# Kernel tuning notes

Measured on AMD Instinct MI355X. Metric: run time of the kernel, lower is better.

## Reference

```python
import jax, jax.numpy as jnp
import numpy as np

HIDDEN = 768
NUM_HEADS = 12
HEAD_DIM = HIDDEN // NUM_HEADS
NUM_SELECTED = 64
SCALE = 1.0 / np.sqrt(HEAD_DIM)


def setup_inputs() -> dict:
    key = jax.random.key(0)
    k0, k1, k2, k3, k4 = jax.random.split(key, 5)
    B, S = 1, 2048
    inputs = jax.random.normal(k0, (B, S, HIDDEN), dtype=jnp.float32)
    # nn.Linear weights, stored as [out, in]; applied as x @ W.T
    Wq = jax.random.normal(k1, (HIDDEN, HIDDEN), dtype=jnp.float32) * 0.02
    Wk = jax.random.normal(k2, (HIDDEN, HIDDEN), dtype=jnp.float32) * 0.02
    Wv = jax.random.normal(k3, (HIDDEN, HIDDEN), dtype=jnp.float32) * 0.02
    Wo = jax.random.normal(k4, (HIDDEN, HIDDEN), dtype=jnp.float32) * 0.02
    return {"inputs": inputs, "Wq": Wq, "Wk": Wk, "Wv": Wv, "Wo": Wo}


def reference(inputs, Wq, Wk, Wv, Wo):
    B, S, H = inputs.shape
    K = NUM_SELECTED
    pos = jnp.arange(S)
    window_starts = jnp.clip(pos + 1 - K, 0, None)                      # [S]
    sel = window_starts[:, None] + jnp.arange(K)[None, :]               # [S, K]
    sel = jnp.clip(sel, 0, S - 1)
    causal_mask = sel <= pos[:, None]                                   # [S, K]

    # Per-token linear projections; gathering after the (per-token) linear is
    # mathematically identical to the original gather-then-project.
    q = inputs @ Wq.T                                                   # [B,S,H]
    k_full = inputs @ Wk.T                                              # [B,S,H]
    v_full = inputs @ Wv.T                                              # [B,S,H]

    k = k_full[:, sel]                                                  # [B,S,K,H]
    v = v_full[:, sel]                                                  # [B,S,K,H]

    q = q.reshape(B, S, NUM_HEADS, HEAD_DIM)                            # [B,S,n,d]
    k = k.reshape(B, S, K, NUM_HEADS, HEAD_DIM)                         # [B,S,K,n,d]
    v = v.reshape(B, S, K, NUM_HEADS, HEAD_DIM)

    scores = jnp.einsum("bsnd,bsknd->bnsk", q, k) * SCALE               # [B,n,S,K]
    scores = jnp.where(causal_mask[None, None], scores, -jnp.inf)
    weights = jax.nn.softmax(scores, axis=-1)                           # [B,n,S,K]

    out = jnp.einsum("bnsk,bsknd->bsnd", weights, v)                    # [B,S,n,d]
    out = out.reshape(B, S, H)
    return out @ Wo.T
```

## Files before the change

### kernel.cpp

```cpp
#include <hip/hip_runtime.h>
#include <stdint.h>

#define S_LEN   2048
#define HIDDEN  768
#define NHEADS  12
#define QKV_LD  2304
#define NW      589824

#define REP_CONV 8

typedef __attribute__((ext_vector_type(8))) short short8;
typedef __attribute__((ext_vector_type(4))) float f32x4;

typedef const __attribute__((address_space(1))) void* gas_ptr;
typedef __attribute__((address_space(3))) void* las_ptr;

__device__ __forceinline__ short f2b(float f) {
    union { float f; uint32_t u; } v; v.f = f;
    uint32_t u = v.u;
    uint32_t r = (u + 0x7FFFu + ((u >> 16) & 1u)) >> 16;
    return (short)r;
}

__global__ __launch_bounds__(256)
void convert_all(const float* __restrict__ X,
                 const float* __restrict__ Wq, const float* __restrict__ Wk,
                 const float* __restrict__ Wv, const float* __restrict__ Wo,
                 short* __restrict__ Xb, short* __restrict__ Wqkvb,
                 short* __restrict__ Wob) {
    const int NX4 = 393216, NW4 = 147456, TOT = 983040;
    for (int rep = 0; rep < REP_CONV; ++rep) {
        for (int idx = blockIdx.x * 256 + threadIdx.x; idx < TOT; idx += 1024 * 256) {
            const float* src; short* dst; int e;
            if (idx < NX4) {
                src = X; dst = Xb; e = idx * 4;
            } else {
                int j = idx - NX4;
                int wb = j / NW4, lb = j % NW4;
                src = wb == 0 ? Wq : wb == 1 ? Wk : wb == 2 ? Wv : Wo;
                dst = wb < 3 ? Wqkvb + wb * NW : Wob;
                e = lb * 4;
            }
            float4 v = *(const float4*)(src + e);
            *(short4*)(dst + e) = make_short4(f2b(v.x), f2b(v.y), f2b(v.z), f2b(v.w));
        }
        asm volatile("" ::: "memory");
    }
}

template<int OUT_BF16>
__device__ __forceinline__ void gemm64x128(const short* __restrict__ A,
    const short* __restrict__ B, void* __restrict__ Cv,
    int bm, int bn, int ldc) {
    __shared__ short sA[2][64 * 64];
    __shared__ short sB[2][128 * 64];

    const int tid = threadIdx.x, lane = tid & 63, w = tid >> 6;
    const int wr = w >> 1, wc = w & 1;

    f32x4 acc[2][4] = {};

    auto stage = [&](int buf, int k0) {
        #pragma unroll
        for (int c = 0; c < 2; ++c) {
            int r = w * 16 + c * 8 + (lane >> 3);
            int scb = ((lane & 7) * 16) ^ ((r & 7) << 4);
            const char* gp = (const char*)(A + (size_t)(bm * 64 + r) * 768 + k0) + scb;
            __builtin_amdgcn_global_load_lds((gas_ptr)gp,
                (las_ptr)((char*)&sA[buf][0] + w * 2048 + c * 1024), 16, 0, 0);
        }
        #pragma unroll
        for (int c = 0; c < 4; ++c) {
            int r = w * 32 + c * 8 + (lane >> 3);
            int scb = ((lane & 7) * 16) ^ ((r & 7) << 4);
            const char* gp = (const char*)(B + (size_t)(bn * 128 + r) * 768 + k0) + scb;
            __builtin_amdgcn_global_load_lds((gas_ptr)gp,
                (las_ptr)((char*)&sB[buf][0] + w * 4096 + c * 1024), 16, 0, 0);
        }
    };

    stage(0, 0);
    __syncthreads();
    int cur = 0;
    for (int t = 0; t < 12; ++t) {
        if (t < 11) stage(cur ^ 1, (t + 1) * 64);
        #pragma unroll
        for (int kh = 0; kh < 2; ++kh) {
            const int kb = kh * 64 + ((lane >> 4) << 4);
            short8 av[2], bv[4];
            #pragma unroll
            for (int mi = 0; mi < 2; ++mi) {
                int row = wr * 32 + mi * 16 + (lane & 15);
                av[mi] = *(const short8*)((const char*)&sA[cur][0] + row * 128 + (kb ^ ((row & 7) << 4)));
            }
            #pragma unroll
            for (int ni = 0; ni < 4; ++ni) {
                int row = wc * 64 + ni * 16 + (lane & 15);
                bv[ni] = *(const short8*)((const char*)&sB[cur][0] + row * 128 + (kb ^ ((row & 7) << 4)));
            }
            #pragma unroll
            for (int mi = 0; mi < 2; ++mi)
                #pragma unroll
                for (int ni = 0; ni < 4; ++ni)
                    acc[mi][ni] = __builtin_amdgcn_mfma_f32_16x16x32_bf16(
                        av[mi], bv[ni], acc[mi][ni], 0, 0, 0);
        }
        __syncthreads();
        cur ^= 1;
    }

    const int crow0 = bm * 64 + wr * 32;
    const int ccol0 = bn * 128 + wc * 64;
    #pragma unroll
    for (int mi = 0; mi < 2; ++mi)
        #pragma unroll
        for (int ni = 0; ni < 4; ++ni)
            #pragma unroll
            for (int r = 0; r < 4; ++r) {
                int grow = crow0 + mi * 16 + ((lane >> 4) << 2) + r;
                int gcol = ccol0 + ni * 16 + (lane & 15);
                if (OUT_BF16)
                    ((short*)Cv)[(size_t)grow * ldc + gcol] = f2b(acc[mi][ni][r]);
                else
                    ((float*)Cv)[(size_t)grow * ldc + gcol] = acc[mi][ni][r];
            }
}

__global__ __launch_bounds__(256)
void gemm_qkv(const short* __restrict__ Xb, const short* __restrict__ Wqkvb,
              short* __restrict__ C) {
    const int x = blockIdx.x & 7, i = blockIdx.x >> 3;
    const int bm = (x >> 1) * 8 + i / 9;
    const int bn = (x & 1) * 9 + i % 9;
    gemm64x128<1>(Xb, Wqkvb, C, bm, bn, QKV_LD);
}

__global__ __launch_bounds__(256)
void gemm_out(const short* __restrict__ A, const short* __restrict__ Wob,
              float* __restrict__ C) {
    const int bid = blockIdx.x;
    const int sw = (bid & 7) * 24 + (bid >> 3);
    gemm64x128<0>(A, Wob, C, sw / 6, sw % 6, HIDDEN);
}

__global__ __launch_bounds__(256)
void attn_mfma(const short* __restrict__ QKV, short* __restrict__ O) {
    __shared__ short sK[128 * 64];
    __shared__ short sVt[64 * 128];
    __shared__ short sP[4][16 * 128];

    const int bid = blockIdx.x;
    const int task = (bid & 7) * 48 + (bid >> 3);
    const int h = task % NHEADS;
    const int s0 = (task / NHEADS) * 64;
    const int tid = threadIdx.x, lane = tid & 63, w = tid >> 6;

    #pragma unroll
    for (int c = 0; c < 4; ++c) {
        int r = (w * 4 + c) * 8 + (lane >> 3);
        int gr = s0 - 64 + r; if (gr < 0) gr = 0;
        int scb = ((lane & 7) * 16) ^ ((r & 7) << 4);
        const char* gp = (const char*)(QKV + (size_t)gr * QKV_LD + 768 + h * 64) + scb;
        __builtin_amdgcn_global_load_lds((gas_ptr)gp,
            (las_ptr)((char*)sK + (w * 4 + c) * 1024), 16, 0, 0);
    }
    {
        const int d0 = (tid & 7) * 8;
        const int kbase = (tid >> 3) * 4;
        short8 v[4];
        #pragma unroll
        for (int i = 0; i < 4; ++i) {
            int gr = s0 - 64 + kbase + i; if (gr < 0) gr = 0;
            v[i] = *(const short8*)(QKV + (size_t)gr * QKV_LD + 1536 + h * 64 + d0);
        }
        #pragma unroll
        for (int j = 0; j < 8; ++j) {
            int row = d0 + j;
            int b = row * 256 + ((kbase * 2) ^ ((row & 7) << 4));
            *(short4*)((char*)sVt + b) = make_short4(v[0][j], v[1][j], v[2][j], v[3][j]);
        }
    }
    const int qrow = w * 16 + (lane & 15);
    short8 qf[2];
    #pragma unroll
    for (int kk = 0; kk < 2; ++kk)
        qf[kk] = *(const short8*)(QKV + (size_t)(s0 + qrow) * QKV_LD + h * 64
                                  + kk * 32 + ((lane >> 4) << 3));
    __syncthreads();

    f32x4 s_acc[8];
    #pragma unroll
    for (int ct = 0; ct < 8; ++ct) {
        s_acc[ct] = (f32x4){0.f, 0.f, 0.f, 0.f};
        int krow = ct * 16 + (lane & 15);
        #pragma unroll
        for (int kk = 0; kk < 2; ++kk) {
            int cb = kk * 64 + ((lane >> 4) << 4);
            short8 kf = *(const short8*)((const char*)sK + krow * 128 + (cb ^ ((krow & 7) << 4)));
            s_acc[ct] = __builtin_amdgcn_mfma_f32_16x16x32_bf16(qf[kk], kf, s_acc[ct], 0, 0, 0);
        }
    }

    const int kcol = lane & 15;
    const int qb = w * 16 + ((lane >> 4) << 2);
    float p[8][4];
    #pragma unroll
    for (int r = 0; r < 4; ++r) {
        int q = qb + r;
        float m = -1e30f;
        #pragma unroll
        for (int ct = 0; ct < 8; ++ct) {
            int kt = ct * 16 + kcol;
            bool valid = (kt > q) && (kt <= q + 64) && (s0 + kt >= 64);
            float sc = valid ? s_acc[ct][r] * 0.125f : -1e30f;
            p[ct][r] = sc;
            m = fmaxf(m, sc);
        }
        #pragma unroll
        for (int off = 1; off < 16; off <<= 1) m = fmaxf(m, __shfl_xor(m, off));
        float sm = 0.f;
        #pragma unroll
        for (int ct = 0; ct < 8; ++ct) {
            float e = __expf(p[ct][r] - m);
            p[ct][r] = e;
            sm += e;
        }
        #pragma unroll
        for (int off = 1; off < 16; off <<= 1) sm += __shfl_xor(sm, off);
        float inv = 1.f / sm;
        #pragma unroll
        for (int ct = 0; ct < 8; ++ct) p[ct][r] *= inv;
    }

    #pragma unroll
    for (int ct = 0; ct < 8; ++ct)
        #pragma unroll
        for (int r = 0; r < 4; ++r) {
            int row = ((lane >> 4) << 2) + r;
            int b = row * 256 + (((ct * 16 + kcol) * 2) ^ ((row & 7) << 4));
            *(short*)((char*)&sP[w][0] + b) = f2b(p[ct][r]);
        }

    short8 pf[4];
    #pragma unroll
    for (int kk = 0; kk < 4; ++kk) {
        int row = lane & 15;
        int cb = kk * 64 + ((lane >> 4) << 4);
        pf[kk] = *(const short8*)((const char*)&sP[w][0] + row * 256 + (cb ^ ((row & 7) << 4)));
    }
    f32x4 o_acc[4];
    #pragma unroll
    for (int nt = 0; nt < 4; ++nt) {
        o_acc[nt] = (f32x4){0.f, 0.f, 0.f, 0.f};
        #pragma unroll
        for (int kk = 0; kk < 4; ++kk) {
            int vrow = nt * 16 + (lane & 15);
            int cb = kk * 64 + ((lane >> 4) << 4);
            short8 vf = *(const short8*)((const char*)sVt + vrow * 256 + (cb ^ ((vrow & 7) << 4)));
            o_acc[nt] = __builtin_amdgcn_mfma_f32_16x16x32_bf16(pf[kk], vf, o_acc[nt], 0, 0, 0);
        }
    }

    #pragma unroll
    for (int nt = 0; nt < 4; ++nt)
        #pragma unroll
        for (int r = 0; r < 4; ++r) {
            int q = s0 + qb + r;
            int dcol = h * 64 + nt * 16 + (lane & 15);
            O[(size_t)q * HIDDEN + dcol] = f2b(o_acc[nt][r]);
        }
}

extern "C" void kernel_launch(void* const* d_in, const int* in_sizes, int n_in,
                              void* d_out, int out_size, void* d_ws, size_t ws_size,
                              hipStream_t stream) {
    const float* X  = (const float*)d_in[0];
    const float* Wq = (const float*)d_in[1];
    const float* Wk = (const float*)d_in[2];
    const float* Wv = (const float*)d_in[3];
    const float* Wo = (const float*)d_in[4];
    float* out = (float*)d_out;

    char* ws = (char*)d_ws;
    short* Xb    = (short*)ws;
    short* Wqkvb = (short*)(ws + 3145728);
    short* Wob   = (short*)(ws + 6684672);
    short* QKVb  = (short*)(ws + 7864320);
    short* Attnb = (short*)(ws + 17301504);

    convert_all<<<1024, 256, 0, stream>>>(X, Wq, Wk, Wv, Wo, Xb, Wqkvb, Wob);
    gemm_qkv<<<576, 256, 0, stream>>>(Xb, Wqkvb, QKVb);
    attn_mfma<<<384, 256, 0, stream>>>(QKVb, Attnb);
    gemm_out<<<192, 256, 0, stream>>>(Attnb, Wob, out);
}
```

Measured before the change: 55.18 us.

## Drop repeated conversion loop, triple-buffer QKV GEMM, retile output GEMM, overlap attention loads

Removes the 8x repetition of the fp32-to-bf16 conversion pass, so the inputs and weights are converted once instead of eight times. The shared GEMM template is split into two kernels. The QKV GEMM gets a three-stage LDS pipeline with explicit vmcnt waits and one barrier per iteration. The output GEMM switches to 64x64 tiles over 384 blocks for better CU coverage. In the attention kernel, the V global loads are issued early and the transposed V is written to LDS after the softmax, so that latency overlaps with the QK^T MFMAs, and s_setprio is raised around the MFMA loops. The hand-written waitcnt counts have to match the number of loads actually in flight, which makes the code fragile.

```diff
diff --git a/kernel.cpp b/kernel.cpp
--- a/kernel.cpp
+++ b/kernel.cpp
@@ -6,8 +6,6 @@
 #define NHEADS  12
 #define QKV_LD  2304
 #define NW      589824
-
-#define REP_CONV 8
 
 typedef __attribute__((ext_vector_type(8))) short short8;
 typedef __attribute__((ext_vector_type(4))) float f32x4;
@@ -29,31 +27,31 @@
                  short* __restrict__ Xb, short* __restrict__ Wqkvb,
                  short* __restrict__ Wob) {
     const int NX4 = 393216, NW4 = 147456, TOT = 983040;
-    for (int rep = 0; rep < REP_CONV; ++rep) {
-        for (int idx = blockIdx.x * 256 + threadIdx.x; idx < TOT; idx += 1024 * 256) {
-            const float* src; short* dst; int e;
-            if (idx < NX4) {
-                src = X; dst = Xb; e = idx * 4;
-            } else {
-                int j = idx - NX4;
-                int wb = j / NW4, lb = j % NW4;
-                src = wb == 0 ? Wq : wb == 1 ? Wk : wb == 2 ? Wv : Wo;
-                dst = wb < 3 ? Wqkvb + wb * NW : Wob;
-                e = lb * 4;
-            }
-            float4 v = *(const float4*)(src + e);
-            *(short4*)(dst + e) = make_short4(f2b(v.x), f2b(v.y), f2b(v.z), f2b(v.w));
-        }
-        asm volatile("" ::: "memory");
-    }
-}
-
-template<int OUT_BF16>
-__device__ __forceinline__ void gemm64x128(const short* __restrict__ A,
-    const short* __restrict__ B, void* __restrict__ Cv,
-    int bm, int bn, int ldc) {
-    __shared__ short sA[2][64 * 64];
-    __shared__ short sB[2][128 * 64];
+    for (int idx = blockIdx.x * 256 + threadIdx.x; idx < TOT; idx += 1024 * 256) {
+        const float* src; short* dst; int e;
+        if (idx < NX4) {
+            src = X; dst = Xb; e = idx * 4;
+        } else {
+            int j = idx - NX4;
+            int wb = j / NW4, lb = j % NW4;
+            src = wb == 0 ? Wq : wb == 1 ? Wk : wb == 2 ? Wv : Wo;
+            dst = wb < 3 ? Wqkvb + wb * NW : Wob;
+            e = lb * 4;
+        }
+        float4 v = *(const float4*)(src + e);
+        *(short4*)(dst + e) = make_short4(f2b(v.x), f2b(v.y), f2b(v.z), f2b(v.w));
+    }
+}
+
+__global__ __launch_bounds__(256)
+void gemm_qkv(const short* __restrict__ A, const short* __restrict__ B,
+              short* __restrict__ C) {
+    __shared__ short sA[3][64 * 64];
+    __shared__ short sB[3][128 * 64];
+
+    const int x = blockIdx.x & 7, i = blockIdx.x >> 3;
+    const int bm = (x >> 1) * 8 + i / 9;
+    const int bn = (x & 1) * 9 + i % 9;
 
     const int tid = threadIdx.x, lane = tid & 63, w = tid >> 6;
     const int wr = w >> 1, wc = w & 1;
@@ -80,10 +78,16 @@
     };
 
     stage(0, 0);
-    __syncthreads();
-    int cur = 0;
+    stage(1, 64);
     for (int t = 0; t < 12; ++t) {
-        if (t < 11) stage(cur ^ 1, (t + 1) * 64);
+        if (t < 11) asm volatile("s_waitcnt vmcnt(6)" ::: "memory");
+        else        asm volatile("s_waitcnt vmcnt(0)" ::: "memory");
+        __builtin_amdgcn_s_barrier();
+        asm volatile("" ::: "memory");
+        if (t < 10) stage((t + 2) % 3, (t + 2) * 64);
+
+        const char* bA = (const char*)&sA[t % 3][0];
+        const char* bB = (const char*)&sB[t % 3][0];
         #pragma unroll
         for (int kh = 0; kh < 2; ++kh) {
             const int kb = kh * 64 + ((lane >> 4) << 4);
@@ -91,12 +95,12 @@
             #pragma unroll
             for (int mi = 0; mi < 2; ++mi) {
                 int row = wr * 32 + mi * 16 + (lane & 15);
-                av[mi] = *(const short8*)((const char*)&sA[cur][0] + row * 128 + (kb ^ ((row & 7) << 4)));
+                av[mi] = *(const short8*)(bA + row * 128 + (kb ^ ((row & 7) << 4)));
             }
             #pragma unroll
             for (int ni = 0; ni < 4; ++ni) {
                 int row = wc * 64 + ni * 16 + (lane & 15);
-                bv[ni] = *(const short8*)((const char*)&sB[cur][0] + row * 128 + (kb ^ ((row & 7) << 4)));
+                bv[ni] = *(const short8*)(bB + row * 128 + (kb ^ ((row & 7) << 4)));
             }
             #pragma unroll
             for (int mi = 0; mi < 2; ++mi)
@@ -105,8 +109,7 @@
                     acc[mi][ni] = __builtin_amdgcn_mfma_f32_16x16x32_bf16(
                         av[mi], bv[ni], acc[mi][ni], 0, 0, 0);
         }
-        __syncthreads();
-        cur ^= 1;
+        asm volatile("" ::: "memory");
     }
 
     const int crow0 = bm * 64 + wr * 32;
@@ -119,28 +122,81 @@
             for (int r = 0; r < 4; ++r) {
                 int grow = crow0 + mi * 16 + ((lane >> 4) << 2) + r;
                 int gcol = ccol0 + ni * 16 + (lane & 15);
-                if (OUT_BF16)
-                    ((short*)Cv)[(size_t)grow * ldc + gcol] = f2b(acc[mi][ni][r]);
-                else
-                    ((float*)Cv)[(size_t)grow * ldc + gcol] = acc[mi][ni][r];
+                C[(size_t)grow * QKV_LD + gcol] = f2b(acc[mi][ni][r]);
             }
 }
 
 __global__ __launch_bounds__(256)
-void gemm_qkv(const short* __restrict__ Xb, const short* __restrict__ Wqkvb,
-              short* __restrict__ C) {
+void gemm_out(const short* __restrict__ A, const short* __restrict__ B,
+              float* __restrict__ C) {
+    __shared__ short sA[2][64 * 64];
+    __shared__ short sB[2][64 * 64];
+
     const int x = blockIdx.x & 7, i = blockIdx.x >> 3;
-    const int bm = (x >> 1) * 8 + i / 9;
-    const int bn = (x & 1) * 9 + i % 9;
-    gemm64x128<1>(Xb, Wqkvb, C, bm, bn, QKV_LD);
-}
-
-__global__ __launch_bounds__(256)
-void gemm_out(const short* __restrict__ A, const short* __restrict__ Wob,
-              float* __restrict__ C) {
-    const int bid = blockIdx.x;
-    const int sw = (bid & 7) * 24 + (bid >> 3);
-    gemm64x128<0>(A, Wob, C, sw / 6, sw % 6, HIDDEN);
+    const int bm = (x >> 1) * 8 + i / 6;
+    const int bn = (x & 1) * 6 + i % 6;
+
+    const int tid = threadIdx.x, lane = tid & 63, w = tid >> 6;
+    const int wr = w >> 1, wc = w & 1;
+
+    f32x4 acc[2][2] = {};
+
+    auto stage = [&](int buf, int k0) {
+        #pragma unroll
+        for (int c = 0; c < 2; ++c) {
+            int r = w * 16 + c * 8 + (lane >> 3);
+            int scb = ((lane & 7) * 16) ^ ((r & 7) << 4);
+            const char* gpA = (const char*)(A + (size_t)(bm * 64 + r) * 768 + k0) + scb;
+            __builtin_amdgcn_global_load_lds((gas_ptr)gpA,
+                (las_ptr)((char*)&sA[buf][0] + w * 2048 + c * 1024), 16, 0, 0);
+            const char* gpB = (const char*)(B + (size_t)(bn * 64 + r) * 768 + k0) + scb;
+            __builtin_amdgcn_global_load_lds((gas_ptr)gpB,
+                (las_ptr)((char*)&sB[buf][0] + w * 2048 + c * 1024), 16, 0, 0);
+        }
+    };
+
+    stage(0, 0);
+    __syncthreads();
+    int cur = 0;
+    for (int t = 0; t < 12; ++t) {
+        if (t < 11) stage(cur ^ 1, (t + 1) * 64);
+        #pragma unroll
+        for (int kh = 0; kh < 2; ++kh) {
+            const int kb = kh * 64 + ((lane >> 4) << 4);
+            short8 av[2], bv[2];
+            #pragma unroll
+            for (int mi = 0; mi < 2; ++mi) {
+                int row = wr * 32 + mi * 16 + (lane & 15);
+                av[mi] = *(const short8*)((const char*)&sA[cur][0] + row * 128 + (kb ^ ((row & 7) << 4)));
+            }
+            #pragma unroll
+            for (int ni = 0; ni < 2; ++ni) {
+                int row = wc * 32 + ni * 16 + (lane & 15);
+                bv[ni] = *(const short8*)((const char*)&sB[cur][0] + row * 128 + (kb ^ ((row & 7) << 4)));
+            }
+            #pragma unroll
+            for (int mi = 0; mi < 2; ++mi)
+                #pragma unroll
+                for (int ni = 0; ni < 2; ++ni)
+                    acc[mi][ni] = __builtin_amdgcn_mfma_f32_16x16x32_bf16(
+                        av[mi], bv[ni], acc[mi][ni], 0, 0, 0);
+        }
+        __syncthreads();
+        cur ^= 1;
+    }
+
+    const int crow0 = bm * 64 + wr * 32;
+    const int ccol0 = bn * 64 + wc * 32;
+    #pragma unroll
+    for (int mi = 0; mi < 2; ++mi)
+        #pragma unroll
+        for (int ni = 0; ni < 2; ++ni)
+            #pragma unroll
+            for (int r = 0; r < 4; ++r) {
+                int grow = crow0 + mi * 16 + ((lane >> 4) << 2) + r;
+                int gcol = ccol0 + ni * 16 + (lane & 15);
+                C[(size_t)grow * HIDDEN + gcol] = acc[mi][ni][r];
+            }
 }
 
 __global__ __launch_bounds__(256)
@@ -164,31 +220,29 @@
         __builtin_amdgcn_global_load_lds((gas_ptr)gp,
             (las_ptr)((char*)sK + (w * 4 + c) * 1024), 16, 0, 0);
     }
-    {
-        const int d0 = (tid & 7) * 8;
-        const int kbase = (tid >> 3) * 4;
-        short8 v[4];
-        #pragma unroll
-        for (int i = 0; i < 4; ++i) {
-            int gr = s0 - 64 + kbase + i; if (gr < 0) gr = 0;
-            v[i] = *(const short8*)(QKV + (size_t)gr * QKV_LD + 1536 + h * 64 + d0);
-        }
-        #pragma unroll
-        for (int j = 0; j < 8; ++j) {
-            int row = d0 + j;
-            int b = row * 256 + ((kbase * 2) ^ ((row & 7) << 4));
-            *(short4*)((char*)sVt + b) = make_short4(v[0][j], v[1][j], v[2][j], v[3][j]);
-        }
-    }
+    __builtin_amdgcn_sched_barrier(0);
+
     const int qrow = w * 16 + (lane & 15);
     short8 qf[2];
     #pragma unroll
     for (int kk = 0; kk < 2; ++kk)
         qf[kk] = *(const short8*)(QKV + (size_t)(s0 + qrow) * QKV_LD + h * 64
                                   + kk * 32 + ((lane >> 4) << 3));
-    __syncthreads();
+    const int d0 = (tid & 7) * 8;
+    const int kbase = (tid >> 3) * 4;
+    short8 v[4];
+    #pragma unroll
+    for (int i = 0; i < 4; ++i) {
+        int gr = s0 - 64 + kbase + i; if (gr < 0) gr = 0;
+        v[i] = *(const short8*)(QKV + (size_t)gr * QKV_LD + 1536 + h * 64 + d0);
+    }
+
+    asm volatile("s_waitcnt vmcnt(6)" ::: "memory");
+    __builtin_amdgcn_s_barrier();
+    __builtin_amdgcn_sched_barrier(0);
 
     f32x4 s_acc[8];
+    __builtin_amdgcn_s_setprio(1);
     #pragma unroll
     for (int ct = 0; ct < 8; ++ct) {
         s_acc[ct] = (f32x4){0.f, 0.f, 0.f, 0.f};
@@ -200,6 +254,7 @@
             s_acc[ct] = __builtin_amdgcn_mfma_f32_16x16x32_bf16(qf[kk], kf, s_acc[ct], 0, 0, 0);
         }
     }
+    __builtin_amdgcn_s_setprio(0);
 
     const int kcol = lane & 15;
     const int qb = w * 16 + ((lane >> 4) << 2);
@@ -233,6 +288,14 @@
     }
 
     #pragma unroll
+    for (int j = 0; j < 8; ++j) {
+        int jj = (j + tid) & 7;
+        int row = d0 + jj;
+        int b = row * 256 + ((kbase * 2) ^ ((row & 7) << 4));
+        *(short4*)((char*)sVt + b) = make_short4(v[0][jj], v[1][jj], v[2][jj], v[3][jj]);
+    }
+
+    #pragma unroll
     for (int ct = 0; ct < 8; ++ct)
         #pragma unroll
         for (int r = 0; r < 4; ++r) {
@@ -241,6 +304,8 @@
             *(short*)((char*)&sP[w][0] + b) = f2b(p[ct][r]);
         }
 
+    __syncthreads();
+
     short8 pf[4];
     #pragma unroll
     for (int kk = 0; kk < 4; ++kk) {
@@ -249,6 +314,7 @@
         pf[kk] = *(const short8*)((const char*)&sP[w][0] + row * 256 + (cb ^ ((row & 7) << 4)));
     }
     f32x4 o_acc[4];
+    __builtin_amdgcn_s_setprio(1);
     #pragma unroll
     for (int nt = 0; nt < 4; ++nt) {
         o_acc[nt] = (f32x4){0.f, 0.f, 0.f, 0.f};
@@ -260,6 +326,7 @@
             o_acc[nt] = __builtin_amdgcn_mfma_f32_16x16x32_bf16(pf[kk], vf, o_acc[nt], 0, 0, 0);
         }
     }
+    __builtin_amdgcn_s_setprio(0);
 
     #pragma unroll
     for (int nt = 0; nt < 4; ++nt)
@@ -291,5 +358,5 @@
     convert_all<<<1024, 256, 0, stream>>>(X, Wq, Wk, Wv, Wo, Xb, Wqkvb, Wob);
     gemm_qkv<<<576, 256, 0, stream>>>(Xb, Wqkvb, QKVb);
     attn_mfma<<<384, 256, 0, stream>>>(QKVb, Attnb);
-    gemm_out<<<192, 256, 0, stream>>>(Attnb, Wob, out);
-}
+    gemm_out<<<384, 256, 0, stream>>>(Attnb, Wob, out);
+}
```

After: 50.04 us. 9.3% less time.
